# Optimization experiments

Measured on AMD Instinct MI355X. Metric: run time of the kernel, lower is better.

Reference implementation:

```python
import jax, jax.numpy as jnp
import numpy as np


def setup_inputs() -> dict:
    key = jax.random.key(0)
    ks = jax.random.split(key, 7)
    B, S, E = 2, 4096, 512
    return {
        "query": jax.random.normal(ks[0], (B, S, E), jnp.float32),
        "key": jax.random.normal(ks[1], (B, S, E), jnp.float32),
        "value": jax.random.normal(ks[2], (B, S, E), jnp.float32),
        "in_proj_weight": jax.random.normal(ks[3], (3 * E, E), jnp.float32) * 0.02,
        "in_proj_bias": jax.random.normal(ks[4], (3 * E,), jnp.float32) * 0.02,
        "out_proj_weight": jax.random.normal(ks[5], (E, E), jnp.float32) * 0.02,
        "out_proj_bias": jax.random.normal(ks[6], (E,), jnp.float32) * 0.02,
        "window_size": 512,
        "stride": 256,
    }


def reference(query, key, value, in_proj_weight, in_proj_bias,
              out_proj_weight, out_proj_bias, window_size, stride):
    B, S, E = query.shape
    H = 8
    hd = E // H
    scale = 1.0 / np.sqrt(hd).astype(np.float32)

    # Project full sequences once (equivalent to projecting each window slice).
    wq, wk, wv = in_proj_weight[:E], in_proj_weight[E:2 * E], in_proj_weight[2 * E:]
    bq, bk, bv = in_proj_bias[:E], in_proj_bias[E:2 * E], in_proj_bias[2 * E:]
    qp = query @ wq.T + bq   # [B,S,E]
    kp = key @ wk.T + bk
    vp = value @ wv.T + bv

    # Overlapping window gather: [nw, W] token indices.
    starts = np.arange(0, S - window_size + 1, stride)
    idx = starts[:, None] + np.arange(window_size)[None, :]  # [nw, W]
    nw, W = idx.shape

    def heads(x):  # [B,S,E] -> [B,nw,W,H,hd]
        return x[:, idx].reshape(B, nw, W, H, hd)

    qh, kh, vh = heads(qp), heads(kp), heads(vp)

    scores = jnp.einsum('bnqhd,bnkhd->bnhqk', qh, kh) * scale  # [B,nw,H,W,W]
    probs = jax.nn.softmax(scores, axis=-1)
    ctx = jnp.einsum('bnhqk,bnkhd->bnqhd', probs, vh)           # [B,nw,W,H,hd]
    ctx = ctx.reshape(B, nw * W, E)                             # concat over windows
    return ctx @ out_proj_weight.T + out_proj_bias              # [B, nw*W, E]
```

## Files before the change

kernel.cpp:

```cpp
#include <hip/hip_runtime.h>
#include <hip/hip_bf16.h>

typedef __bf16 bf16x8 __attribute__((ext_vector_type(8)));
typedef float f32x4 __attribute__((ext_vector_type(4)));
typedef float f32x16 __attribute__((ext_vector_type(16)));

__device__ __forceinline__ ushort f2bf(float f) {
  union { float f; unsigned u; } x; x.f = f;
  unsigned r = x.u + 0x7fffu + ((x.u >> 16) & 1u);
  return (ushort)(r >> 16);
}

__device__ __forceinline__ void gld_lds16(const void* g, void* l) {
  __builtin_amdgcn_global_load_lds(
      (const __attribute__((address_space(1))) void*)g,
      (__attribute__((address_space(3))) void*)l, 16, 0, 0);
}

__global__ __launch_bounds__(256) void k_cvt_w(
    const float* __restrict__ wi, const float* __restrict__ wo,
    ushort* __restrict__ dst) {
  const int NWI = 196608, NWO = 65536;
  const int total = NWI + NWO;
  int i = blockIdx.x * 256 + threadIdx.x;
  int stride = gridDim.x * 256;
  for (; i < total; i += stride) {
    const float* s; int j;
    if (i < NWI) { s = wi; j = i; }
    else         { s = wo; j = i - NWI; }
    float4 val = reinterpret_cast<const float4*>(s)[j];
    ushort4 o;
    o.x = f2bf(val.x); o.y = f2bf(val.y); o.z = f2bf(val.z); o.w = f2bf(val.w);
    reinterpret_cast<ushort4*>(dst)[i] = o;
  }
}

#define GK 512
#define GN 512

__global__ __launch_bounds__(256) void k_gemm_qkv(
    const float* __restrict__ za0, const float* __restrict__ za1,
    const float* __restrict__ za2,
    const ushort* __restrict__ Btbase,
    const float* __restrict__ biasbase,
    ushort* __restrict__ Cbase, float qs)
{
  int z = blockIdx.z;
  const float* A32 = (z == 0) ? za0 : (z == 1) ? za1 : za2;
  const ushort* Bt = Btbase + (size_t)262144 * z;
  const float* bias = biasbase + 512 * z;
  float osc = (z == 0) ? qs : 1.0f;

  __shared__ ushort As[2][4096];
  __shared__ ushort Bs[2][4096];

  int tid = threadIdx.x;
  int wv = tid >> 6, ln = tid & 63;
  int l15 = ln & 15, lg = ln >> 4;
  int wm = wv >> 1, wn = wv & 1;
  int m0 = blockIdx.x * 128, n0 = blockIdx.y * 128;

  int row_s = tid >> 1, kh = (tid & 1) * 16;
  const float* aP = A32 + (size_t)(m0 + row_s) * GK + kh;
  int ldsOff = row_s * 32 + kh;

  f32x4 acc[4][4] = {};

  {
#pragma unroll
    for (int h2 = 0; h2 < 2; ++h2) {
      int c = h2 * 256 + wv * 64 + ln;
      int row = c >> 2, kc = (c & 3) * 8;
      gld_lds16(Bt + (size_t)(n0 + row) * GK + kc,
                (char*)&Bs[0][0] + (h2 * 256 + wv * 64) * 16);
    }
    float4 f0 = reinterpret_cast<const float4*>(aP)[0];
    float4 f1 = reinterpret_cast<const float4*>(aP)[1];
    float4 f2 = reinterpret_cast<const float4*>(aP)[2];
    float4 f3 = reinterpret_cast<const float4*>(aP)[3];
    uint w0, w1, w2, w3, w4, w5, w6, w7;
    asm("v_cvt_pk_bf16_f32 %0, %1, %2" : "=v"(w0) : "v"(f0.x), "v"(f0.y));
    asm("v_cvt_pk_bf16_f32 %0, %1, %2" : "=v"(w1) : "v"(f0.z), "v"(f0.w));
    asm("v_cvt_pk_bf16_f32 %0, %1, %2" : "=v"(w2) : "v"(f1.x), "v"(f1.y));
    asm("v_cvt_pk_bf16_f32 %0, %1, %2" : "=v"(w3) : "v"(f1.z), "v"(f1.w));
    asm("v_cvt_pk_bf16_f32 %0, %1, %2" : "=v"(w4) : "v"(f2.x), "v"(f2.y));
    asm("v_cvt_pk_bf16_f32 %0, %1, %2" : "=v"(w5) : "v"(f2.z), "v"(f2.w));
    asm("v_cvt_pk_bf16_f32 %0, %1, %2" : "=v"(w6) : "v"(f3.x), "v"(f3.y));
    asm("v_cvt_pk_bf16_f32 %0, %1, %2" : "=v"(w7) : "v"(f3.z), "v"(f3.w));
    uint4 p0; p0.x = w0; p0.y = w1; p0.z = w2; p0.w = w3;
    uint4 p1; p1.x = w4; p1.y = w5; p1.z = w6; p1.w = w7;
    reinterpret_cast<uint4*>(&As[0][ldsOff])[0] = p0;
    reinterpret_cast<uint4*>(&As[0][ldsOff + 8])[0] = p1;
  }
  __syncthreads();

  for (int kt = 0; kt < 16; ++kt) {
    int cur = kt & 1, nxt = cur ^ 1;
    float4 f0, f1, f2, f3;
    bool pf = (kt < 15);
    if (pf) {
#pragma unroll
      for (int h2 = 0; h2 < 2; ++h2) {
        int c = h2 * 256 + wv * 64 + ln;
        int row = c >> 2, kc = (c & 3) * 8;
        gld_lds16(Bt + (size_t)(n0 + row) * GK + (kt + 1) * 32 + kc,
                  (char*)&Bs[nxt][0] + (h2 * 256 + wv * 64) * 16);
      }
      const float* ap = aP + (kt + 1) * 32;
      f0 = reinterpret_cast<const float4*>(ap)[0];
      f1 = reinterpret_cast<const float4*>(ap)[1];
      f2 = reinterpret_cast<const float4*>(ap)[2];
      f3 = reinterpret_cast<const float4*>(ap)[3];
    }

    bf16x8 af[4], bf4[4];
#pragma unroll
    for (int mf = 0; mf < 4; ++mf)
      af[mf] = *reinterpret_cast<const bf16x8*>(&As[cur][(wm * 64 + mf * 16 + l15) * 32 + lg * 8]);
#pragma unroll
    for (int nf = 0; nf < 4; ++nf)
      bf4[nf] = *reinterpret_cast<const bf16x8*>(&Bs[cur][(wn * 64 + nf * 16 + l15) * 32 + lg * 8]);
#pragma unroll
    for (int mf = 0; mf < 4; ++mf)
#pragma unroll
      for (int nf = 0; nf < 4; ++nf)
        acc[mf][nf] = __builtin_amdgcn_mfma_f32_16x16x32_bf16(af[mf], bf4[nf], acc[mf][nf], 0, 0, 0);

    if (pf) {
      uint w0, w1, w2, w3, w4, w5, w6, w7;
      asm("v_cvt_pk_bf16_f32 %0, %1, %2" : "=v"(w0) : "v"(f0.x), "v"(f0.y));
      asm("v_cvt_pk_bf16_f32 %0, %1, %2" : "=v"(w1) : "v"(f0.z), "v"(f0.w));
      asm("v_cvt_pk_bf16_f32 %0, %1, %2" : "=v"(w2) : "v"(f1.x), "v"(f1.y));
      asm("v_cvt_pk_bf16_f32 %0, %1, %2" : "=v"(w3) : "v"(f1.z), "v"(f1.w));
      asm("v_cvt_pk_bf16_f32 %0, %1, %2" : "=v"(w4) : "v"(f2.x), "v"(f2.y));
      asm("v_cvt_pk_bf16_f32 %0, %1, %2" : "=v"(w5) : "v"(f2.z), "v"(f2.w));
      asm("v_cvt_pk_bf16_f32 %0, %1, %2" : "=v"(w6) : "v"(f3.x), "v"(f3.y));
      asm("v_cvt_pk_bf16_f32 %0, %1, %2" : "=v"(w7) : "v"(f3.z), "v"(f3.w));
      uint4 p0; p0.x = w0; p0.y = w1; p0.z = w2; p0.w = w3;
      uint4 p1; p1.x = w4; p1.y = w5; p1.z = w6; p1.w = w7;
      reinterpret_cast<uint4*>(&As[nxt][ldsOff])[0] = p0;
      reinterpret_cast<uint4*>(&As[nxt][ldsOff + 8])[0] = p1;
    }
    __syncthreads();
  }

#pragma unroll
  for (int mf = 0; mf < 4; ++mf)
#pragma unroll
    for (int nf = 0; nf < 4; ++nf)
#pragma unroll
      for (int r = 0; r < 4; ++r) {
        int rr = m0 + wm * 64 + mf * 16 + lg * 4 + r;
        int cc = n0 + wn * 64 + nf * 16 + l15;
        float v = (acc[mf][nf][r] + bias[cc]) * osc;
        (Cbase + (size_t)4194304 * z)[(size_t)rr * GN + cc] = f2bf(v);
      }
}

__global__ __launch_bounds__(256) void k_gemm_out(
    const ushort* __restrict__ Ab, const ushort* __restrict__ Bt,
    const float* __restrict__ bias, float* __restrict__ C)
{
  __shared__ ushort As[128 * 32];
  __shared__ ushort Bs[128 * 32];

  int tid = threadIdx.x;
  int wv = tid >> 6, ln = tid & 63;
  int l15 = ln & 15, lg = ln >> 4;
  int wm = wv >> 1, wn = wv & 1;
  int m0 = blockIdx.x * 128, n0 = blockIdx.y * 128;

  f32x4 acc[4][4] = {};

  for (int kt = 0; kt < GK / 32; ++kt) {
    __syncthreads();
#pragma unroll
    for (int h2 = 0; h2 < 2; ++h2) {
      int c = h2 * 256 + wv * 64 + ln;
      int row = c >> 2, kc = (c & 3) * 8;
      gld_lds16(Ab + (size_t)(m0 + row) * GK + kt * 32 + kc,
                (char*)As + (h2 * 256 + wv * 64) * 16);
      gld_lds16(Bt + (size_t)(n0 + row) * GK + kt * 32 + kc,
                (char*)Bs + (h2 * 256 + wv * 64) * 16);
    }
    __syncthreads();
    bf16x8 af[4], bf4[4];
#pragma unroll
    for (int mf = 0; mf < 4; ++mf)
      af[mf] = *reinterpret_cast<const bf16x8*>(&As[(wm * 64 + mf * 16 + l15) * 32 + lg * 8]);
#pragma unroll
    for (int nf = 0; nf < 4; ++nf)
      bf4[nf] = *reinterpret_cast<const bf16x8*>(&Bs[(wn * 64 + nf * 16 + l15) * 32 + lg * 8]);
#pragma unroll
    for (int mf = 0; mf < 4; ++mf)
#pragma unroll
      for (int nf = 0; nf < 4; ++nf)
        acc[mf][nf] = __builtin_amdgcn_mfma_f32_16x16x32_bf16(af[mf], bf4[nf], acc[mf][nf], 0, 0, 0);
  }

#pragma unroll
  for (int mf = 0; mf < 4; ++mf)
#pragma unroll
    for (int nf = 0; nf < 4; ++nf)
#pragma unroll
      for (int r = 0; r < 4; ++r) {
        int rr = m0 + wm * 64 + mf * 16 + lg * 4 + r;
        int cc = n0 + wn * 64 + nf * 16 + l15;
        C[(size_t)rr * GN + cc] = acc[mf][nf][r] + bias[cc];
      }
}

__global__ __launch_bounds__(256, 2) void k_attn(
    const ushort* __restrict__ qp, const ushort* __restrict__ kp,
    const ushort* __restrict__ vp, ushort* __restrict__ ctx)
{
  const int E = 512, SEQ = 4096;
  int bid0 = blockIdx.x;
  int bid = (bid0 & 7) * 60 + (bid0 >> 3);
  int qh = bid & 1;
  int h = (bid >> 1) & 7;
  int n = (bid >> 4) % 15;
  int b = bid / 240;
  int start = n * 256;

  int tid = threadIdx.x;
  int w = tid >> 6, ln = tid & 63;
  int l31 = ln & 31, hi = ln >> 5;

  size_t base = ((size_t)(b * SEQ + start)) * E + h * 64;
  const ushort* Kw = kp + base;
  const ushort* Vw = vp + base;
  const ushort* Qw = qp + base;

  __shared__ ushort Vt[32768];

  {
    int sk = (tid & 63) * 8;
    int sd = (tid >> 6) * 16;
    const ushort* src = Vw + (size_t)sk * E + sd;
    union { uint4 q[2]; ushort u[16]; } R0, R1, R2, R3, R4, R5, R6, R7;
    R0.q[0] = *(const uint4*)(src + 0 * E); R0.q[1] = *(const uint4*)(src + 0 * E + 8);
    R1.q[0] = *(const uint4*)(src + 1 * E); R1.q[1] = *(const uint4*)(src + 1 * E + 8);
    R2.q[0] = *(const uint4*)(src + 2 * E); R2.q[1] = *(const uint4*)(src + 2 * E + 8);
    R3.q[0] = *(const uint4*)(src + 3 * E); R3.q[1] = *(const uint4*)(src + 3 * E + 8);
    R4.q[0] = *(const uint4*)(src + 4 * E); R4.q[1] = *(const uint4*)(src + 4 * E + 8);
    R5.q[0] = *(const uint4*)(src + 5 * E); R5.q[1] = *(const uint4*)(src + 5 * E + 8);
    R6.q[0] = *(const uint4*)(src + 6 * E); R6.q[1] = *(const uint4*)(src + 6 * E + 8);
    R7.q[0] = *(const uint4*)(src + 7 * E); R7.q[1] = *(const uint4*)(src + 7 * E + 8);
#pragma unroll
    for (int d0 = 0; d0 < 16; ++d0) {
      int d = sd + d0;
      uint4 val;
      val.x = (uint)R0.u[d0] | ((uint)R1.u[d0] << 16);
      val.y = (uint)R2.u[d0] | ((uint)R3.u[d0] << 16);
      val.z = (uint)R4.u[d0] | ((uint)R5.u[d0] << 16);
      val.w = (uint)R6.u[d0] | ((uint)R7.u[d0] << 16);
      int off = d * 1024 + ((sk * 2) ^ ((d & 7) << 4));
      *(uint4*)((char*)Vt + off) = val;
    }
  }
  __syncthreads();

  int q0 = qh * 256 + w * 64;

  bf16x8 qa0, qa1, qa2, qa3, qb0, qb1, qb2, qb3;
  {
    const ushort* qra = Qw + (size_t)(q0 + l31) * E + hi * 8;
    const ushort* qrb = qra + (size_t)32 * E;
    qa0 = *reinterpret_cast<const bf16x8*>(qra + 0);
    qa1 = *reinterpret_cast<const bf16x8*>(qra + 16);
    qa2 = *reinterpret_cast<const bf16x8*>(qra + 32);
    qa3 = *reinterpret_cast<const bf16x8*>(qra + 48);
    qb0 = *reinterpret_cast<const bf16x8*>(qrb + 0);
    qb1 = *reinterpret_cast<const bf16x8*>(qrb + 16);
    qb2 = *reinterpret_cast<const bf16x8*>(qrb + 32);
    qb3 = *reinterpret_cast<const bf16x8*>(qrb + 48);
  }

  f32x16 ca0 = {}, ca1 = {}, cb0_ = {}, cb1_ = {};
  float psa = 0.f, psb = 0.f;
  const char* lb = (const char*)Vt;

#pragma unroll
  for (int kb = 0; kb < 16; ++kb) {
    bf16x8 kf0, kf1, kf2, kf3;
    {
      const ushort* kr = Kw + (size_t)(kb * 32 + l31) * E + hi * 8;
      kf0 = *reinterpret_cast<const bf16x8*>(kr + 0);
      kf1 = *reinterpret_cast<const bf16x8*>(kr + 16);
      kf2 = *reinterpret_cast<const bf16x8*>(kr + 32);
      kf3 = *reinterpret_cast<const bf16x8*>(kr + 48);
    }
    bf16x8 vb00, vb01, vb10, vb11;
    {
      int row = l31, rowh = 32 + l31;
      int cb0 = kb * 64 + hi * 16;
      int cb1 = cb0 + 32;
      int xr0 = (row & 7) << 4;
      vb00 = *reinterpret_cast<const bf16x8*>(lb + row * 1024 + (cb0 ^ xr0));
      vb01 = *reinterpret_cast<const bf16x8*>(lb + rowh * 1024 + (cb0 ^ xr0));
      vb10 = *reinterpret_cast<const bf16x8*>(lb + row * 1024 + (cb1 ^ xr0));
      vb11 = *reinterpret_cast<const bf16x8*>(lb + rowh * 1024 + (cb1 ^ xr0));
    }

    f32x16 s1 = {}, s2 = {};
    __builtin_amdgcn_s_setprio(1);
    s1 = __builtin_amdgcn_mfma_f32_32x32x16_bf16(kf0, qa0, s1, 0, 0, 0);
    s2 = __builtin_amdgcn_mfma_f32_32x32x16_bf16(kf0, qb0, s2, 0, 0, 0);
    s1 = __builtin_amdgcn_mfma_f32_32x32x16_bf16(kf1, qa1, s1, 0, 0, 0);
    s2 = __builtin_amdgcn_mfma_f32_32x32x16_bf16(kf1, qb1, s2, 0, 0, 0);
    s1 = __builtin_amdgcn_mfma_f32_32x32x16_bf16(kf2, qa2, s1, 0, 0, 0);
    s2 = __builtin_amdgcn_mfma_f32_32x32x16_bf16(kf2, qb2, s2, 0, 0, 0);
    s1 = __builtin_amdgcn_mfma_f32_32x32x16_bf16(kf3, qa3, s1, 0, 0, 0);
    s2 = __builtin_amdgcn_mfma_f32_32x32x16_bf16(kf3, qb3, s2, 0, 0, 0);
    __builtin_amdgcn_s_setprio(0);

#pragma unroll
    for (int r = 0; r < 16; ++r) s1[r] = __builtin_amdgcn_exp2f(s1[r]);
#pragma unroll
    for (int r = 0; r < 16; ++r) s2[r] = __builtin_amdgcn_exp2f(s2[r]);
    {
      float t0 = (s1[0] + s1[1]) + (s1[2] + s1[3]);
      float t1 = (s1[4] + s1[5]) + (s1[6] + s1[7]);
      float t2 = (s1[8] + s1[9]) + (s1[10] + s1[11]);
      float t3 = (s1[12] + s1[13]) + (s1[14] + s1[15]);
      psa += (t0 + t1) + (t2 + t3);
      float u0 = (s2[0] + s2[1]) + (s2[2] + s2[3]);
      float u1 = (s2[4] + s2[5]) + (s2[6] + s2[7]);
      float u2 = (s2[8] + s2[9]) + (s2[10] + s2[11]);
      float u3 = (s2[12] + s2[13]) + (s2[14] + s2[15]);
      psb += (u0 + u1) + (u2 + u3);
    }

    uint a0, a1, a2, a3, a4, a5, a6, a7;
    asm("v_cvt_pk_bf16_f32 %0, %1, %2" : "=v"(a0) : "v"(s1[0]),  "v"(s1[1]));
    asm("v_cvt_pk_bf16_f32 %0, %1, %2" : "=v"(a1) : "v"(s1[2]),  "v"(s1[3]));
    asm("v_cvt_pk_bf16_f32 %0, %1, %2" : "=v"(a2) : "v"(s1[4]),  "v"(s1[5]));
    asm("v_cvt_pk_bf16_f32 %0, %1, %2" : "=v"(a3) : "v"(s1[6]),  "v"(s1[7]));
    asm("v_cvt_pk_bf16_f32 %0, %1, %2" : "=v"(a4) : "v"(s1[8]),  "v"(s1[9]));
    asm("v_cvt_pk_bf16_f32 %0, %1, %2" : "=v"(a5) : "v"(s1[10]), "v"(s1[11]));
    asm("v_cvt_pk_bf16_f32 %0, %1, %2" : "=v"(a6) : "v"(s1[12]), "v"(s1[13]));
    asm("v_cvt_pk_bf16_f32 %0, %1, %2" : "=v"(a7) : "v"(s1[14]), "v"(s1[15]));
    asm("v_permlane32_swap_b32 %0, %1" : "+v"(a0), "+v"(a2));
    asm("v_permlane32_swap_b32 %0, %1" : "+v"(a1), "+v"(a3));
    asm("v_permlane32_swap_b32 %0, %1" : "+v"(a4), "+v"(a6));
    asm("v_permlane32_swap_b32 %0, %1" : "+v"(a5), "+v"(a7));
    uint b0, b1, b2, b3, b4, b5, b6, b7;
    asm("v_cvt_pk_bf16_f32 %0, %1, %2" : "=v"(b0) : "v"(s2[0]),  "v"(s2[1]));
    asm("v_cvt_pk_bf16_f32 %0, %1, %2" : "=v"(b1) : "v"(s2[2]),  "v"(s2[3]));
    asm("v_cvt_pk_bf16_f32 %0, %1, %2" : "=v"(b2) : "v"(s2[4]),  "v"(s2[5]));
    asm("v_cvt_pk_bf16_f32 %0, %1, %2" : "=v"(b3) : "v"(s2[6]),  "v"(s2[7]));
    asm("v_cvt_pk_bf16_f32 %0, %1, %2" : "=v"(b4) : "v"(s2[8]),  "v"(s2[9]));
    asm("v_cvt_pk_bf16_f32 %0, %1, %2" : "=v"(b5) : "v"(s2[10]), "v"(s2[11]));
    asm("v_cvt_pk_bf16_f32 %0, %1, %2" : "=v"(b6) : "v"(s2[12]), "v"(s2[13]));
    asm("v_cvt_pk_bf16_f32 %0, %1, %2" : "=v"(b7) : "v"(s2[14]), "v"(s2[15]));
    asm("v_permlane32_swap_b32 %0, %1" : "+v"(b0), "+v"(b2));
    asm("v_permlane32_swap_b32 %0, %1" : "+v"(b1), "+v"(b3));
    asm("v_permlane32_swap_b32 %0, %1" : "+v"(b4), "+v"(b6));
    asm("v_permlane32_swap_b32 %0, %1" : "+v"(b5), "+v"(b7));
    union { uint u[4]; bf16x8 v; } A1, A2, B1, B2;
    A1.u[0] = a0; A1.u[1] = a1; A1.u[2] = a2; A1.u[3] = a3;
    A2.u[0] = a4; A2.u[1] = a5; A2.u[2] = a6; A2.u[3] = a7;
    B1.u[0] = b0; B1.u[1] = b1; B1.u[2] = b2; B1.u[3] = b3;
    B2.u[0] = b4; B2.u[1] = b5; B2.u[2] = b6; B2.u[3] = b7;

    __builtin_amdgcn_s_setprio(1);
    ca0  = __builtin_amdgcn_mfma_f32_32x32x16_bf16(A1.v, vb00, ca0, 0, 0, 0);
    cb0_ = __builtin_amdgcn_mfma_f32_32x32x16_bf16(B1.v, vb00, cb0_, 0, 0, 0);
    ca1  = __builtin_amdgcn_mfma_f32_32x32x16_bf16(A1.v, vb01, ca1, 0, 0, 0);
    cb1_ = __builtin_amdgcn_mfma_f32_32x32x16_bf16(B1.v, vb01, cb1_, 0, 0, 0);
    ca0  = __builtin_amdgcn_mfma_f32_32x32x16_bf16(A2.v, vb10, ca0, 0, 0, 0);
    cb0_ = __builtin_amdgcn_mfma_f32_32x32x16_bf16(B2.v, vb10, cb0_, 0, 0, 0);
    ca1  = __builtin_amdgcn_mfma_f32_32x32x16_bf16(A2.v, vb11, ca1, 0, 0, 0);
    cb1_ = __builtin_amdgcn_mfma_f32_32x32x16_bf16(B2.v, vb11, cb1_, 0, 0, 0);
    __builtin_amdgcn_s_setprio(0);
  }

  psa += __shfl_xor(psa, 32);
  psb += __shfl_xor(psb, 32);
  float ria = 1.0f / psa;
  float rib = 1.0f / psb;
  size_t orow0 = (size_t)b * 7680 + (size_t)n * 512 + q0;
#pragma unroll
  for (int r = 0; r < 16; ++r) {
    int qrel = (r & 3) + 8 * (r >> 2) + 4 * hi;
    float r1 = __shfl(ria, qrel);
    float r2 = __shfl(rib, qrel);
    ushort* dA = ctx + (orow0 + qrel) * E + h * 64 + l31;
    ushort* dB = ctx + (orow0 + 32 + qrel) * E + h * 64 + l31;
    dA[0]  = f2bf(ca0[r] * r1);
    dA[32] = f2bf(ca1[r] * r1);
    dB[0]  = f2bf(cb0_[r] * r2);
    dB[32] = f2bf(cb1_[r] * r2);
  }
}

extern "C" void kernel_launch(void* const* d_in, const int* in_sizes, int n_in,
                              void* d_out, int out_size, void* d_ws, size_t ws_size,
                              hipStream_t stream) {
  const float* query = (const float*)d_in[0];
  const float* key   = (const float*)d_in[1];
  const float* value = (const float*)d_in[2];
  const float* ipw   = (const float*)d_in[3];
  const float* ipb   = (const float*)d_in[4];
  const float* opw   = (const float*)d_in[5];
  const float* opb   = (const float*)d_in[6];

  ushort* wib = (ushort*)d_ws;
  ushort* wob = wib + 786432;
  ushort* qp  = wob + 262144;
  ushort* kp  = qp  + 4194304;
  ushort* vp  = kp  + 4194304;
  ushort* ctx = vp  + 4194304;

  const float SC = 0.125f * 1.44269504088896340736f;

  k_cvt_w<<<512, 256, 0, stream>>>(ipw, opw, wib);

  k_gemm_qkv<<<dim3(64, 4, 3), 256, 0, stream>>>(
      query, key, value, wib, ipb, qp, SC);

  k_attn<<<480, 256, 0, stream>>>(qp, kp, vp, ctx);

  k_gemm_out<<<dim3(120, 4, 1), 256, 0, stream>>>(
      ctx, wob, opb, (float*)d_out);
}
```

Baseline: 83.24 us.

## Load fp32 A tiles directly to LDS with XOR swizzle, drop double buffering

The QKV projection GEMM now streams the fp32 activation tile straight into LDS with global_load_lds, using an XOR swizzle to avoid bank conflicts. The bf16 conversion moves to after the LDS read, into the fragment load. The register-staged, double-buffered prefetch is replaced by a single-buffered load, sync, compute loop, which removes overlap between global loads and MFMA work. LDS use for A doubles per buffer, and each tile is converted twice, once by each wn warp.

```diff
diff --git a/kernel.cpp b/kernel.cpp
--- a/kernel.cpp
+++ b/kernel.cpp
@@ -51,8 +51,8 @@
   const float* bias = biasbase + 512 * z;
   float osc = (z == 0) ? qs : 1.0f;
 
-  __shared__ ushort As[2][4096];
-  __shared__ ushort Bs[2][4096];
+  __shared__ float  As[128 * 32];
+  __shared__ ushort Bs[128 * 32];
 
   int tid = threadIdx.x;
   int wv = tid >> 6, ln = tid & 63;
@@ -60,88 +60,53 @@
   int wm = wv >> 1, wn = wv & 1;
   int m0 = blockIdx.x * 128, n0 = blockIdx.y * 128;
 
-  int row_s = tid >> 1, kh = (tid & 1) * 16;
-  const float* aP = A32 + (size_t)(m0 + row_s) * GK + kh;
-  int ldsOff = row_s * 32 + kh;
-
   f32x4 acc[4][4] = {};
 
-  {
+  for (int kt = 0; kt < 16; ++kt) {
+    __syncthreads();
+#pragma unroll
+    for (int it = 0; it < 4; ++it) {
+      int s = it * 256 + tid;
+      int row = s >> 3;
+      int cs = (s & 7) * 16;
+      int gofs = (cs ^ ((row & 7) << 4)) >> 2;
+      gld_lds16(A32 + (size_t)(m0 + row) * GK + kt * 32 + gofs,
+                (char*)As + (it * 256 + wv * 64) * 16);
+    }
 #pragma unroll
     for (int h2 = 0; h2 < 2; ++h2) {
       int c = h2 * 256 + wv * 64 + ln;
       int row = c >> 2, kc = (c & 3) * 8;
-      gld_lds16(Bt + (size_t)(n0 + row) * GK + kc,
-                (char*)&Bs[0][0] + (h2 * 256 + wv * 64) * 16);
-    }
-    float4 f0 = reinterpret_cast<const float4*>(aP)[0];
-    float4 f1 = reinterpret_cast<const float4*>(aP)[1];
-    float4 f2 = reinterpret_cast<const float4*>(aP)[2];
-    float4 f3 = reinterpret_cast<const float4*>(aP)[3];
-    uint w0, w1, w2, w3, w4, w5, w6, w7;
-    asm("v_cvt_pk_bf16_f32 %0, %1, %2" : "=v"(w0) : "v"(f0.x), "v"(f0.y));
-    asm("v_cvt_pk_bf16_f32 %0, %1, %2" : "=v"(w1) : "v"(f0.z), "v"(f0.w));
-    asm("v_cvt_pk_bf16_f32 %0, %1, %2" : "=v"(w2) : "v"(f1.x), "v"(f1.y));
-    asm("v_cvt_pk_bf16_f32 %0, %1, %2" : "=v"(w3) : "v"(f1.z), "v"(f1.w));
-    asm("v_cvt_pk_bf16_f32 %0, %1, %2" : "=v"(w4) : "v"(f2.x), "v"(f2.y));
-    asm("v_cvt_pk_bf16_f32 %0, %1, %2" : "=v"(w5) : "v"(f2.z), "v"(f2.w));
-    asm("v_cvt_pk_bf16_f32 %0, %1, %2" : "=v"(w6) : "v"(f3.x), "v"(f3.y));
-    asm("v_cvt_pk_bf16_f32 %0, %1, %2" : "=v"(w7) : "v"(f3.z), "v"(f3.w));
-    uint4 p0; p0.x = w0; p0.y = w1; p0.z = w2; p0.w = w3;
-    uint4 p1; p1.x = w4; p1.y = w5; p1.z = w6; p1.w = w7;
-    reinterpret_cast<uint4*>(&As[0][ldsOff])[0] = p0;
-    reinterpret_cast<uint4*>(&As[0][ldsOff + 8])[0] = p1;
-  }
-  __syncthreads();
-
-  for (int kt = 0; kt < 16; ++kt) {
-    int cur = kt & 1, nxt = cur ^ 1;
-    float4 f0, f1, f2, f3;
-    bool pf = (kt < 15);
-    if (pf) {
-#pragma unroll
-      for (int h2 = 0; h2 < 2; ++h2) {
-        int c = h2 * 256 + wv * 64 + ln;
-        int row = c >> 2, kc = (c & 3) * 8;
-        gld_lds16(Bt + (size_t)(n0 + row) * GK + (kt + 1) * 32 + kc,
-                  (char*)&Bs[nxt][0] + (h2 * 256 + wv * 64) * 16);
-      }
-      const float* ap = aP + (kt + 1) * 32;
-      f0 = reinterpret_cast<const float4*>(ap)[0];
-      f1 = reinterpret_cast<const float4*>(ap)[1];
-      f2 = reinterpret_cast<const float4*>(ap)[2];
-      f3 = reinterpret_cast<const float4*>(ap)[3];
-    }
+      gld_lds16(Bt + (size_t)(n0 + row) * GK + kt * 32 + kc,
+                (char*)Bs + (h2 * 256 + wv * 64) * 16);
+    }
+    __syncthreads();
 
     bf16x8 af[4], bf4[4];
 #pragma unroll
-    for (int mf = 0; mf < 4; ++mf)
-      af[mf] = *reinterpret_cast<const bf16x8*>(&As[cur][(wm * 64 + mf * 16 + l15) * 32 + lg * 8]);
+    for (int mf = 0; mf < 4; ++mf) {
+      int row = wm * 64 + mf * 16 + l15;
+      int xr = (row & 7) << 4;
+      const char* rb = (const char*)As + row * 128;
+      float4 x0 = *reinterpret_cast<const float4*>(rb + ((lg * 32) ^ xr));
+      float4 x1 = *reinterpret_cast<const float4*>(rb + (((lg * 32) + 16) ^ xr));
+      uint w0, w1, w2, w3;
+      asm("v_cvt_pk_bf16_f32 %0, %1, %2" : "=v"(w0) : "v"(x0.x), "v"(x0.y));
+      asm("v_cvt_pk_bf16_f32 %0, %1, %2" : "=v"(w1) : "v"(x0.z), "v"(x0.w));
+      asm("v_cvt_pk_bf16_f32 %0, %1, %2" : "=v"(w2) : "v"(x1.x), "v"(x1.y));
+      asm("v_cvt_pk_bf16_f32 %0, %1, %2" : "=v"(w3) : "v"(x1.z), "v"(x1.w));
+      union { uint u[4]; bf16x8 v; } t;
+      t.u[0] = w0; t.u[1] = w1; t.u[2] = w2; t.u[3] = w3;
+      af[mf] = t.v;
+    }
 #pragma unroll
     for (int nf = 0; nf < 4; ++nf)
-      bf4[nf] = *reinterpret_cast<const bf16x8*>(&Bs[cur][(wn * 64 + nf * 16 + l15) * 32 + lg * 8]);
+      bf4[nf] = *reinterpret_cast<const bf16x8*>(&Bs[(wn * 64 + nf * 16 + l15) * 32 + lg * 8]);
 #pragma unroll
     for (int mf = 0; mf < 4; ++mf)
 #pragma unroll
       for (int nf = 0; nf < 4; ++nf)
         acc[mf][nf] = __builtin_amdgcn_mfma_f32_16x16x32_bf16(af[mf], bf4[nf], acc[mf][nf], 0, 0, 0);
-
-    if (pf) {
-      uint w0, w1, w2, w3, w4, w5, w6, w7;
-      asm("v_cvt_pk_bf16_f32 %0, %1, %2" : "=v"(w0) : "v"(f0.x), "v"(f0.y));
-      asm("v_cvt_pk_bf16_f32 %0, %1, %2" : "=v"(w1) : "v"(f0.z), "v"(f0.w));
-      asm("v_cvt_pk_bf16_f32 %0, %1, %2" : "=v"(w2) : "v"(f1.x), "v"(f1.y));
-      asm("v_cvt_pk_bf16_f32 %0, %1, %2" : "=v"(w3) : "v"(f1.z), "v"(f1.w));
-      asm("v_cvt_pk_bf16_f32 %0, %1, %2" : "=v"(w4) : "v"(f2.x), "v"(f2.y));
-      asm("v_cvt_pk_bf16_f32 %0, %1, %2" : "=v"(w5) : "v"(f2.z), "v"(f2.w));
-      asm("v_cvt_pk_bf16_f32 %0, %1, %2" : "=v"(w6) : "v"(f3.x), "v"(f3.y));
-      asm("v_cvt_pk_bf16_f32 %0, %1, %2" : "=v"(w7) : "v"(f3.z), "v"(f3.w));
-      uint4 p0; p0.x = w0; p0.y = w1; p0.z = w2; p0.w = w3;
-      uint4 p1; p1.x = w4; p1.y = w5; p1.z = w6; p1.w = w7;
-      reinterpret_cast<uint4*>(&As[nxt][ldsOff])[0] = p0;
-      reinterpret_cast<uint4*>(&As[nxt][ldsOff + 8])[0] = p1;
-    }
-    __syncthreads();
   }
 
 #pragma unroll
```

After: 84.24 us. No clear change (+1.2%).
